# Kernel tuning notes

Hardware: AMD Instinct MI355X
Metric: run time of the kernel (lower is better)

Reference implementation:

```python
import jax, jax.numpy as jnp
import numpy as np

HEADS = 16

def setup_inputs() -> dict:
    key = jax.random.key(0)
    k1, k2, k3 = jax.random.split(key, 3)
    T, B, E = 2048, 4, 1024
    query = jax.random.normal(k1, (T, B, E), dtype=jnp.float32)
    in_proj_weight = jax.random.normal(k2, (3 * E, E), dtype=jnp.float32) * (E ** -0.5)
    out_proj_weight = jax.random.normal(k3, (E, E), dtype=jnp.float32) * (E ** -0.5)
    return {"query": query, "in_proj_weight": in_proj_weight, "out_proj_weight": out_proj_weight}

def reference(query, in_proj_weight, out_proj_weight):
    # query: [T, B, E] (time-first, as in apex SelfMultiheadAttn)
    T, B, E = query.shape
    H = HEADS
    D = E // H
    scale = D ** -0.5
    # fused in-projection: x @ W_in^T -> [T, B, 3E]
    qkv = jnp.einsum('tbe,fe->tbf', query, in_proj_weight)
    q, k, v = jnp.split(qkv, 3, axis=-1)
    # [T, B, E] -> [B, H, T, D]
    def to_bhtd(x):
        return x.reshape(T, B, H, D).transpose(1, 2, 0, 3)
    q = to_bhtd(q) * scale
    k = to_bhtd(k)
    v = to_bhtd(v)
    scores = jnp.einsum('bhqd,bhkd->bhqk', q, k)  # [B, H, T, T]
    # causal (mask_future_timesteps=True) time mask
    causal = jnp.tril(jnp.ones((T, T), dtype=bool))
    scores = jnp.where(causal, scores, jnp.finfo(scores.dtype).min)
    attn = jax.nn.softmax(scores, axis=-1)
    # dropout_prob = 0.0 -> identity
    ctx = jnp.einsum('bhqk,bhkd->bhqd', attn, v)  # [B, H, T, D]
    ctx = ctx.transpose(2, 0, 1, 3).reshape(T, B, E)
    out = jnp.einsum('tbe,fe->tbf', ctx, out_proj_weight)
    return out
```

## Files before the change

### kernel.cpp

```cpp
#include <hip/hip_runtime.h>


typedef float  f32x4  __attribute__((ext_vector_type(4)));
typedef short  s16x8  __attribute__((ext_vector_type(8)));
typedef __bf16 bf16x8 __attribute__((ext_vector_type(8)));

#define T_DIM 2048
#define B_DIM 4
#define E_DIM 1024
#define PLANE (T_DIM * 64)

__device__ inline unsigned short f2bf(float f) {
  return (unsigned short)((__builtin_bit_cast(unsigned int, f) + 0x8000u) >> 16);
}

__device__ inline f32x4 mfma16(s16x8 a, s16x8 b, f32x4 c) {
  return __builtin_amdgcn_mfma_f32_16x16x32_bf16(
      __builtin_bit_cast(bf16x8, a), __builtin_bit_cast(bf16x8, b), c, 0, 0, 0);
}

__device__ inline void gl2lds16(const unsigned short* g, unsigned short* l) {
  __builtin_amdgcn_global_load_lds(
      (__attribute__((address_space(1))) unsigned int*)g,
      (__attribute__((address_space(3))) unsigned int*)l, 16, 0, 0);
}

__device__ inline unsigned packbf(float a, float b) {
  return __builtin_amdgcn_perm(__builtin_bit_cast(unsigned, b),
                               __builtin_bit_cast(unsigned, a), 0x07060302u);
}

__global__ __launch_bounds__(256)
void cvt_all(const float* __restrict__ q, const float* __restrict__ wi,
             const float* __restrict__ wo, unsigned short* __restrict__ xb,
             unsigned short* __restrict__ wib, unsigned short* __restrict__ wob,
             float qs, int do_wout) {
  int blk = blockIdx.x;
  const float* src;
  unsigned short* dst;
  int i;
  float sc = 1.0f;
  if (blk < 8192) {
    src = q; dst = xb; i = blk * 256 + threadIdx.x;
  } else if (blk < 11264) {
    src = wi; dst = wib; i = (blk - 8192) * 256 + threadIdx.x;
    if (i < (E_DIM * E_DIM / 4)) sc = qs;
  } else {
    if (!do_wout) return;
    src = wo; dst = wob; i = (blk - 11264) * 256 + threadIdx.x;
  }
  float4 v = ((const float4*)src)[i];
  ushort4 o;
  o.x = f2bf(v.x * sc); o.y = f2bf(v.y * sc);
  o.z = f2bf(v.z * sc); o.w = f2bf(v.w * sc);
  ((ushort4*)dst)[i] = o;
}

__global__ __launch_bounds__(256)
void cvt_bf16(const float* __restrict__ in, unsigned short* __restrict__ out,
              int n4) {
  int i = blockIdx.x * 256 + threadIdx.x;
  if (i >= n4) return;
  float4 v = ((const float4*)in)[i];
  ushort4 o;
  o.x = f2bf(v.x); o.y = f2bf(v.y); o.z = f2bf(v.z); o.w = f2bf(v.w);
  ((ushort4*)out)[i] = o;
}

__global__ __launch_bounds__(256, 2)
void gemm256(const unsigned short* __restrict__ A,
             const unsigned short* __restrict__ Bw,
             unsigned short* __restrict__ Cq, int K) {
  __shared__ __attribute__((aligned(16))) unsigned short As[256 * 64];
  __shared__ __attribute__((aligned(16))) unsigned short Bs[128 * 64];

  const int tid = threadIdx.x, lane = tid & 63, w = tid >> 6;
  const int row16 = lane & 15, quad = lane >> 4;
  const int m0 = blockIdx.y * 256, n0 = blockIdx.x * 128;
  const int wm = (w & 1) * 128, wn = (w >> 1) * 64;
  const int srow = lane >> 3;
  const int jsw = (lane & 7) ^ srow;
  const int sw7 = row16 & 7;

  f32x4 acc[8][4];
  for (int i = 0; i < 8; ++i)
    for (int j = 0; j < 4; ++j) acc[i][j] = (f32x4){0.f, 0.f, 0.f, 0.f};

  for (int k0 = 0; k0 < K; k0 += 64) {
    for (int i2 = 0; i2 < 8; ++i2) {
      int ia = w * 8 + i2;
      int r = ia * 8 + srow;
      gl2lds16(A + (size_t)(m0 + r) * K + k0 + jsw * 8, &As[ia * 512]);
    }
    for (int i2 = 0; i2 < 4; ++i2) {
      int ib = w * 4 + i2;
      int r = ib * 8 + srow;
      gl2lds16(Bw + (size_t)(n0 + r) * K + k0 + jsw * 8, &Bs[ib * 512]);
    }
    __syncthreads();
    for (int kk = 0; kk < 2; ++kk) {
      s16x8 af[8], bfr[4];
      for (int mi = 0; mi < 8; ++mi)
        af[mi] = *(const s16x8*)&As[(wm + mi * 16 + row16) * 64 +
                                    (((kk * 4 + quad) ^ sw7) * 8)];
      for (int ni = 0; ni < 4; ++ni)
        bfr[ni] = *(const s16x8*)&Bs[(wn + ni * 16 + row16) * 64 +
                                     (((kk * 4 + quad) ^ sw7) * 8)];
      for (int mi = 0; mi < 8; ++mi)
        for (int ni = 0; ni < 4; ++ni)
          acc[mi][ni] = mfma16(af[mi], bfr[ni], acc[mi][ni]);
    }
    __syncthreads();
  }

  if (n0 >= 2048) {
    const int hw = ((n0 & 1023) >> 6) + (w >> 1);
    const int tg0 = (m0 >> 2) + (w & 1) * 32;
    unsigned short* tb = &As[w * 2560];
    for (int bb = 0; bb < 4; ++bb) {
      for (int mi = 0; mi < 8; ++mi)
        for (int ni = 0; ni < 4; ++ni)
          tb[(ni * 16 + row16) * 40 + mi * 4 + quad] = f2bf(acc[mi][ni][bb]);
      asm volatile("s_waitcnt lgkmcnt(0)" ::: "memory");
      unsigned short* vp = Cq + (size_t)(128 + bb * 16 + hw) * PLANE;
      for (int it = 0; it < 4; ++it) {
        int dd = it * 16 + (lane >> 2);
        int tl = (lane & 3) * 8;
        s16x8 v = *(const s16x8*)&tb[dd * 40 + tl];
        *(s16x8*)(vp + (size_t)dd * T_DIM + tg0 + tl) = v;
      }
      asm volatile("s_waitcnt lgkmcnt(0)" ::: "memory");
    }
  } else {
    for (int mi = 0; mi < 8; ++mi)
      for (int ni = 0; ni < 4; ++ni)
        for (int r = 0; r < 4; ++r) {
          int m = m0 + wm + mi * 16 + quad * 4 + r;
          int n = n0 + wn + ni * 16 + row16;
          int t = m >> 2, bb = m & 3;
          int which = n >> 10, hh = (n >> 6) & 15, dd = n & 63;
          Cq[(size_t)(which * 64 + bb * 16 + hh) * PLANE + (size_t)t * 64 + dd] =
              f2bf(acc[mi][ni][r]);
        }
  }
}

__global__ __launch_bounds__(256)
void gemm128(const unsigned short* __restrict__ A,
             const unsigned short* __restrict__ Bw,
             float* __restrict__ Cf, int N, int K) {
  __shared__ __attribute__((aligned(16))) unsigned short As[128 * 64];
  __shared__ __attribute__((aligned(16))) unsigned short Bs[128 * 64];

  const int tid = threadIdx.x, lane = tid & 63, w = tid >> 6;
  const int row16 = lane & 15, quad = lane >> 4;
  const int m0 = blockIdx.y * 128, n0 = blockIdx.x * 128;
  const int wm = (w & 1) * 64, wn = (w >> 1) * 64;
  const int srow = lane >> 3;
  const int jsw = (lane & 7) ^ srow;
  const int sw7 = row16 & 7;

  f32x4 acc[4][4];
  for (int i = 0; i < 4; ++i)
    for (int j = 0; j < 4; ++j) acc[i][j] = (f32x4){0.f, 0.f, 0.f, 0.f};

  for (int k0 = 0; k0 < K; k0 += 64) {
    for (int i = 0; i < 4; ++i) {
      int ia = i * 4 + w;
      int r = ia * 8 + srow;
      gl2lds16(A  + (size_t)(m0 + r) * K + k0 + jsw * 8, &As[ia * 512]);
      gl2lds16(Bw + (size_t)(n0 + r) * K + k0 + jsw * 8, &Bs[ia * 512]);
    }
    __syncthreads();
    for (int kk = 0; kk < 2; ++kk) {
      s16x8 af[4], bfr[4];
      for (int mi = 0; mi < 4; ++mi)
        af[mi] = *(const s16x8*)&As[(wm + mi * 16 + row16) * 64 +
                                    (((kk * 4 + quad) ^ sw7) * 8)];
      for (int ni = 0; ni < 4; ++ni)
        bfr[ni] = *(const s16x8*)&Bs[(wn + ni * 16 + row16) * 64 +
                                     (((kk * 4 + quad) ^ sw7) * 8)];
      for (int mi = 0; mi < 4; ++mi)
        for (int ni = 0; ni < 4; ++ni)
          acc[mi][ni] = mfma16(af[mi], bfr[ni], acc[mi][ni]);
    }
    __syncthreads();
  }

  for (int mi = 0; mi < 4; ++mi)
    for (int ni = 0; ni < 4; ++ni)
      for (int r = 0; r < 4; ++r) {
        int m = m0 + wm + mi * 16 + quad * 4 + r;
        int n = n0 + wn + ni * 16 + row16;
        Cf[(size_t)m * N + n] = acc[mi][ni][r];
      }
}

__global__ __launch_bounds__(256)
void attn_fwd(const unsigned short* __restrict__ qkv,
              unsigned short* __restrict__ ctx) {
  __shared__ __attribute__((aligned(16))) unsigned short Ks[2][4096];
  __shared__ __attribute__((aligned(16))) unsigned short Vs[2][4096];
  __shared__ __attribute__((aligned(16))) unsigned short Ps[4][2048];

  const int tid = threadIdx.x, lane = tid & 63, w = tid >> 6;
  const int row16 = lane & 15, quad = lane >> 4;
  const int bh = blockIdx.x;
  const int p  = blockIdx.y;
  const int b = bh >> 4, h = bh & 15;

  const unsigned short* Qg = qkv + (size_t)bh * PLANE;
  const unsigned short* Kg = qkv + (size_t)(64 + bh) * PLANE;
  const unsigned short* Vt = qkv + (size_t)(128 + bh) * PLANE;

  const int r8 = lane >> 3;
  const int jsw = (lane & 7) ^ r8;
  const int sw7 = row16 & 7;

  auto stage = [&](int c, int buf) {
    for (int i2 = 0; i2 < 2; ++i2) {
      int i = w + i2 * 4;
      int r = i * 8 + r8;
      gl2lds16(Kg + (size_t)(c * 64 + r) * 64 + jsw * 8, &Ks[buf][i * 512]);
      gl2lds16(Vt + (size_t)r * T_DIM + c * 64 + jsw * 8, &Vs[buf][i * 512]);
    }
  };

  for (int half = 0; half < 2; ++half) {
    const int qt = half ? p : (15 - p);
    const int q0w = qt * 128 + w * 32;
    const int cmax = 2 * qt + 1;
    const int dc = 2 * qt + (w >> 1);

    s16x8 qb[2][2];
    for (int nq = 0; nq < 2; ++nq)
      for (int s = 0; s < 2; ++s)
        qb[nq][s] = *(const s16x8*)(Qg + (size_t)(q0w + nq * 16 + row16) * 64 +
                                    s * 32 + quad * 8);

    f32x4 O[4][2];
    for (int md = 0; md < 4; ++md)
      for (int nq = 0; nq < 2; ++nq) O[md][nq] = (f32x4){0.f, 0.f, 0.f, 0.f};
    float lp[2] = {0.f, 0.f};

    stage(0, 0);
    stage(1, 1);

    for (int c = 0; c <= cmax; ++c) {
      const int buf = c & 1;
      if (c < cmax) asm volatile("s_waitcnt vmcnt(4)" ::: "memory");
      else          asm volatile("s_waitcnt vmcnt(0)" ::: "memory");
      __builtin_amdgcn_s_barrier();

      if (c <= dc) {
        f32x4 S[4][2];
        for (int nt = 0; nt < 4; ++nt)
          for (int nq = 0; nq < 2; ++nq) S[nt][nq] = (f32x4){0.f, 0.f, 0.f, 0.f};
        __builtin_amdgcn_s_setprio(1);
        for (int nt = 0; nt < 4; ++nt)
          for (int s = 0; s < 2; ++s) {
            s16x8 ka = *(const s16x8*)&Ks[buf][(nt * 16 + row16) * 64 +
                                              (((s * 4 + quad) ^ sw7) * 8)];
            for (int nq = 0; nq < 2; ++nq)
              S[nt][nq] = mfma16(ka, qb[nq][s], S[nt][nq]);
          }
        __builtin_amdgcn_s_setprio(0);

        auto softmax_store = [&](bool diagm) {
          for (int nq = 0; nq < 2; ++nq) {
            const int qg = q0w + nq * 16 + row16;
            for (int nt = 0; nt < 4; ++nt) {
              float pv[4];
              for (int r = 0; r < 4; ++r) {
                pv[r] = __builtin_amdgcn_exp2f(S[nt][nq][r]);
                if (diagm && (c * 64 + nt * 16 + quad * 4 + r) > qg) pv[r] = 0.f;
                lp[nq] += pv[r];
              }
              int qr = nq * 16 + row16;
              int pos = (nt * 2 + (quad >> 1)) ^ sw7;
              *(uint2*)&Ps[w][qr * 64 + pos * 8 + (quad & 1) * 4] =
                  make_uint2(packbf(pv[0], pv[1]), packbf(pv[2], pv[3]));
            }
          }
        };
        if (c == dc) softmax_store(true); else softmax_store(false);
        asm volatile("s_waitcnt lgkmcnt(0)" ::: "memory");

        __builtin_amdgcn_s_setprio(1);
        for (int sk = 0; sk < 2; ++sk) {
          s16x8 pb[2];
          for (int nq = 0; nq < 2; ++nq)
            pb[nq] = *(const s16x8*)&Ps[w][(nq * 16 + row16) * 64 +
                                           (((sk * 4 + quad) ^ sw7) * 8)];
          for (int md = 0; md < 4; ++md) {
            s16x8 va = *(const s16x8*)&Vs[buf][(md * 16 + row16) * 64 +
                                              (((sk * 4 + quad) ^ sw7) * 8)];
            for (int nq = 0; nq < 2; ++nq)
              O[md][nq] = mfma16(va, pb[nq], O[md][nq]);
          }
        }
        __builtin_amdgcn_s_setprio(0);
      }

      __builtin_amdgcn_s_barrier();
      if (c + 2 <= cmax) stage(c + 2, buf);
    }

    for (int nq = 0; nq < 2; ++nq) {
      float s = lp[nq];
      s += __shfl_xor(s, 16);
      s += __shfl_xor(s, 32);
      float inv = 1.f / s;
      const int t = q0w + nq * 16 + row16;
      for (int md = 0; md < 4; ++md) {
        unsigned lo = packbf(O[md][nq][0] * inv, O[md][nq][1] * inv);
        unsigned hi = packbf(O[md][nq][2] * inv, O[md][nq][3] * inv);
        *(uint2*)&ctx[((size_t)t * B_DIM + b) * E_DIM + h * 64 + md * 16 +
                      quad * 4] = make_uint2(lo, hi);
      }
    }
  }
}

extern "C" void kernel_launch(void* const* d_in, const int* in_sizes, int n_in,
                              void* d_out, int out_size, void* d_ws,
                              size_t ws_size, hipStream_t stream) {
  const float* query = (const float*)d_in[0];
  const float* win   = (const float*)d_in[1];
  const float* wout  = (const float*)d_in[2];
  float* out = (float*)d_out;

  const size_t qkv_el = (size_t)3 * 64 * PLANE;
  const size_t ctx_el = (size_t)T_DIM * B_DIM * E_DIM;

  unsigned short* qkvb = (unsigned short*)d_ws;
  unsigned short* ctxb = qkvb + qkv_el;
  unsigned short* xb   = ctxb;
  unsigned short* winb = (unsigned short*)d_out;

  const bool big_ws = ws_size >= (qkv_el + ctx_el + (size_t)E_DIM * E_DIM) * 2;
  unsigned short* woutb = big_ws ? (ctxb + ctx_el) : qkvb;

  const float QSCALE = 0.18033688011112042f;

  cvt_all<<<big_ws ? 12288 : 11264, 256, 0, stream>>>(
      query, win, wout, xb, winb, woutb, QSCALE, big_ws ? 1 : 0);
  gemm256<<<dim3(3072 / 128, 8192 / 256), 256, 0, stream>>>(xb, winb, qkvb,
                                                            1024);
  attn_fwd<<<dim3(64, 8), 256, 0, stream>>>(qkvb, ctxb);
  if (!big_ws)
    cvt_bf16<<<1024, 256, 0, stream>>>(wout, woutb, (1024 * 1024) / 4);
  gemm128<<<dim3(8, 64), 256, 0, stream>>>(ctxb, woutb, out, 1024, 1024);
}
```

Baseline: 232.5 us.

## Split attention work across 8 waves with 16 query rows each

```diff
diff --git a/kernel.cpp b/kernel.cpp
--- a/kernel.cpp
+++ b/kernel.cpp
@@ -196,12 +196,12 @@
       }
 }
 
-__global__ __launch_bounds__(256)
+__global__ __launch_bounds__(512, 4)
 void attn_fwd(const unsigned short* __restrict__ qkv,
               unsigned short* __restrict__ ctx) {
   __shared__ __attribute__((aligned(16))) unsigned short Ks[2][4096];
   __shared__ __attribute__((aligned(16))) unsigned short Vs[2][4096];
-  __shared__ __attribute__((aligned(16))) unsigned short Ps[4][2048];
+  __shared__ __attribute__((aligned(16))) unsigned short Ps[8][1024];
 
   const int tid = threadIdx.x, lane = tid & 63, w = tid >> 6;
   const int row16 = lane & 15, quad = lane >> 4;
@@ -218,69 +218,59 @@
   const int sw7 = row16 & 7;
 
   auto stage = [&](int c, int buf) {
-    for (int i2 = 0; i2 < 2; ++i2) {
-      int i = w + i2 * 4;
-      int r = i * 8 + r8;
-      gl2lds16(Kg + (size_t)(c * 64 + r) * 64 + jsw * 8, &Ks[buf][i * 512]);
-      gl2lds16(Vt + (size_t)r * T_DIM + c * 64 + jsw * 8, &Vs[buf][i * 512]);
-    }
+    int r = w * 8 + r8;
+    gl2lds16(Kg + (size_t)(c * 64 + r) * 64 + jsw * 8, &Ks[buf][w * 512]);
+    gl2lds16(Vt + (size_t)r * T_DIM + c * 64 + jsw * 8, &Vs[buf][w * 512]);
   };
 
   for (int half = 0; half < 2; ++half) {
     const int qt = half ? p : (15 - p);
-    const int q0w = qt * 128 + w * 32;
+    const int q0w = qt * 128 + w * 16;
     const int cmax = 2 * qt + 1;
-    const int dc = 2 * qt + (w >> 1);
-
-    s16x8 qb[2][2];
-    for (int nq = 0; nq < 2; ++nq)
-      for (int s = 0; s < 2; ++s)
-        qb[nq][s] = *(const s16x8*)(Qg + (size_t)(q0w + nq * 16 + row16) * 64 +
-                                    s * 32 + quad * 8);
-
-    f32x4 O[4][2];
-    for (int md = 0; md < 4; ++md)
-      for (int nq = 0; nq < 2; ++nq) O[md][nq] = (f32x4){0.f, 0.f, 0.f, 0.f};
-    float lp[2] = {0.f, 0.f};
+    const int dc = 2 * qt + (w >> 2);
+
+    s16x8 qb[2];
+    for (int s = 0; s < 2; ++s)
+      qb[s] = *(const s16x8*)(Qg + (size_t)(q0w + row16) * 64 + s * 32 +
+                              quad * 8);
+
+    f32x4 O[4];
+    for (int md = 0; md < 4; ++md) O[md] = (f32x4){0.f, 0.f, 0.f, 0.f};
+    float lp = 0.f;
 
     stage(0, 0);
     stage(1, 1);
 
     for (int c = 0; c <= cmax; ++c) {
       const int buf = c & 1;
-      if (c < cmax) asm volatile("s_waitcnt vmcnt(4)" ::: "memory");
+      if (c < cmax) asm volatile("s_waitcnt vmcnt(2)" ::: "memory");
       else          asm volatile("s_waitcnt vmcnt(0)" ::: "memory");
       __builtin_amdgcn_s_barrier();
 
       if (c <= dc) {
-        f32x4 S[4][2];
-        for (int nt = 0; nt < 4; ++nt)
-          for (int nq = 0; nq < 2; ++nq) S[nt][nq] = (f32x4){0.f, 0.f, 0.f, 0.f};
+        f32x4 S[4];
+        for (int nt = 0; nt < 4; ++nt) S[nt] = (f32x4){0.f, 0.f, 0.f, 0.f};
         __builtin_amdgcn_s_setprio(1);
         for (int nt = 0; nt < 4; ++nt)
           for (int s = 0; s < 2; ++s) {
             s16x8 ka = *(const s16x8*)&Ks[buf][(nt * 16 + row16) * 64 +
                                               (((s * 4 + quad) ^ sw7) * 8)];
-            for (int nq = 0; nq < 2; ++nq)
-              S[nt][nq] = mfma16(ka, qb[nq][s], S[nt][nq]);
+            S[nt] = mfma16(ka, qb[s], S[nt]);
           }
         __builtin_amdgcn_s_setprio(0);
 
+        const int qg = q0w + row16;
         auto softmax_store = [&](bool diagm) {
-          for (int nq = 0; nq < 2; ++nq) {
-            const int qg = q0w + nq * 16 + row16;
-            for (int nt = 0; nt < 4; ++nt) {
-              float pv[4];
-              for (int r = 0; r < 4; ++r) {
-                pv[r] = __builtin_amdgcn_exp2f(S[nt][nq][r]);
-                if (diagm && (c * 64 + nt * 16 + quad * 4 + r) > qg) pv[r] = 0.f;
-                lp[nq] += pv[r];
-              }
-              int qr = nq * 16 + row16;
-              int pos = (nt * 2 + (quad >> 1)) ^ sw7;
-              *(uint2*)&Ps[w][qr * 64 + pos * 8 + (quad & 1) * 4] =
-                  make_uint2(packbf(pv[0], pv[1]), packbf(pv[2], pv[3]));
+          for (int nt = 0; nt < 4; ++nt) {
+            float pv[4];
+            for (int r = 0; r < 4; ++r) {
+              pv[r] = __builtin_amdgcn_exp2f(S[nt][r]);
+              if (diagm && (c * 64 + nt * 16 + quad * 4 + r) > qg) pv[r] = 0.f;
+              lp += pv[r];
             }
+            int pos = (nt * 2 + (quad >> 1)) ^ sw7;
+            *(uint2*)&Ps[w][row16 * 64 + pos * 8 + (quad & 1) * 4] =
+                make_uint2(packbf(pv[0], pv[1]), packbf(pv[2], pv[3]));
           }
         };
         if (c == dc) softmax_store(true); else softmax_store(false);
@@ -288,15 +278,12 @@
 
         __builtin_amdgcn_s_setprio(1);
         for (int sk = 0; sk < 2; ++sk) {
-          s16x8 pb[2];
-          for (int nq = 0; nq < 2; ++nq)
-            pb[nq] = *(const s16x8*)&Ps[w][(nq * 16 + row16) * 64 +
-                                           (((sk * 4 + quad) ^ sw7) * 8)];
+          s16x8 pb = *(const s16x8*)&Ps[w][row16 * 64 +
+                                          (((sk * 4 + quad) ^ sw7) * 8)];
           for (int md = 0; md < 4; ++md) {
             s16x8 va = *(const s16x8*)&Vs[buf][(md * 16 + row16) * 64 +
                                               (((sk * 4 + quad) ^ sw7) * 8)];
-            for (int nq = 0; nq < 2; ++nq)
-              O[md][nq] = mfma16(va, pb[nq], O[md][nq]);
+            O[md] = mfma16(va, pb, O[md]);
           }
         }
         __builtin_amdgcn_s_setprio(0);
@@ -306,15 +293,15 @@
       if (c + 2 <= cmax) stage(c + 2, buf);
     }
 
-    for (int nq = 0; nq < 2; ++nq) {
-      float s = lp[nq];
+    {
+      float s = lp;
       s += __shfl_xor(s, 16);
       s += __shfl_xor(s, 32);
       float inv = 1.f / s;
-      const int t = q0w + nq * 16 + row16;
+      const int t = q0w + row16;
       for (int md = 0; md < 4; ++md) {
-        unsigned lo = packbf(O[md][nq][0] * inv, O[md][nq][1] * inv);
-        unsigned hi = packbf(O[md][nq][2] * inv, O[md][nq][3] * inv);
+        unsigned lo = packbf(O[md][0] * inv, O[md][1] * inv);
+        unsigned hi = packbf(O[md][2] * inv, O[md][3] * inv);
         *(uint2*)&ctx[((size_t)t * B_DIM + b) * E_DIM + h * 64 + md * 16 +
                       quad * 4] = make_uint2(lo, hi);
       }
@@ -347,7 +334,7 @@
       query, win, wout, xb, winb, woutb, QSCALE, big_ws ? 1 : 0);
   gemm256<<<dim3(3072 / 128, 8192 / 256), 256, 0, stream>>>(xb, winb, qkvb,
                                                             1024);
-  attn_fwd<<<dim3(64, 8), 256, 0, stream>>>(qkvb, ctxb);
+  attn_fwd<<<dim3(64, 8), 512, 0, stream>>>(qkvb, ctxb);
   if (!big_ws)
     cvt_bf16<<<1024, 256, 0, stream>>>(wout, woutb, (1024 * 1024) / 4);
   gemm128<<<dim3(8, 64), 256, 0, stream>>>(ctxb, woutb, out, 1024, 1024);
```

New measurement: 223.8 us. 3.7% less time.
